# Optimization experiments

Measured on AMD Instinct MI355X. Metric: run time of the kernel, lower is better.

## Reference

```python
import jax, jax.numpy as jnp
import numpy as np

NUM_ANCHORS = 400_000
NUM_GTS = 64
NUM_CLASSES = 1
TOPK = 10
ALPHA = 1.0
BETA = 6.0
IMG = 640.0


def setup_inputs() -> dict:
    key = jax.random.key(0)
    k1, k2, k3, k4, k5, k6 = jax.random.split(key, 6)
    # anchor points uniformly over the image plane
    anc_points = jax.random.uniform(k1, (NUM_ANCHORS, 2), jnp.float32, 0.0, IMG)
    # predicted boxes: centered near the anchor point, valid xyxy
    pd_wh = jax.random.uniform(k2, (NUM_ANCHORS, 2), jnp.float32, 8.0, 96.0)
    pd_bboxes = jnp.concatenate([anc_points - pd_wh * 0.5, anc_points + pd_wh * 0.5], axis=-1)
    # predicted class scores in [0, 1] (post-sigmoid)
    pd_scores = jax.random.uniform(k3, (NUM_ANCHORS, NUM_CLASSES), jnp.float32)
    # GT boxes: random centers / sizes, valid xyxy
    gt_c = jax.random.uniform(k4, (NUM_GTS, 2), jnp.float32, 64.0, IMG - 64.0)
    gt_wh = jax.random.uniform(k5, (NUM_GTS, 2), jnp.float32, 16.0, 128.0)
    gt_bboxes = jnp.concatenate([gt_c - gt_wh * 0.5, gt_c + gt_wh * 0.5], axis=-1)
    gt_labels = jax.random.randint(k6, (NUM_GTS,), 0, NUM_CLASSES, dtype=jnp.int32)
    return {
        "pd_scores": pd_scores,
        "pd_bboxes": pd_bboxes,
        "anc_points": anc_points,
        "gt_labels": gt_labels,
        "gt_bboxes": gt_bboxes,
    }


def _box_iou(b1, b2):
    # b1: [A,4] xyxy, b2: [G,4] xyxy -> [A,G] pairwise IoU (torchvision box_iou math)
    lt = jnp.maximum(b1[:, None, :2], b2[None, :, :2])  # [A,G,2]
    rb = jnp.minimum(b1[:, None, 2:], b2[None, :, 2:])  # [A,G,2]
    wh = jnp.clip(rb - lt, 0.0)
    inter = wh[..., 0] * wh[..., 1]                      # [A,G]
    area1 = (b1[:, 2] - b1[:, 0]) * (b1[:, 3] - b1[:, 1])
    area2 = (b2[:, 2] - b2[:, 0]) * (b2[:, 3] - b2[:, 1])
    return inter / (area1[:, None] + area2[None, :] - inter)


def reference(pd_scores, pd_bboxes, anc_points, gt_labels, gt_bboxes):
    A = anc_points.shape[0]
    G = gt_bboxes.shape[0]
    # is anchor point inside each GT box -> [A,G] bool
    x, y = anc_points[:, 0:1], anc_points[:, 1:2]
    is_in_gts = ((x >= gt_bboxes[None, :, 0]) & (x <= gt_bboxes[None, :, 2]) &
                 (y >= gt_bboxes[None, :, 1]) & (y <= gt_bboxes[None, :, 3]))
    # Original gathers candidate anchors (inside >=1 GT) then computes metrics.
    # Equivalent dense form: non-candidates have is_in_gts row all-False so their
    # alignment metric is 0 for every GT and they are filtered by metric>0 below.
    iou = _box_iou(pd_bboxes, gt_bboxes)                         # [A,G]
    cls_scores = pd_scores[:, gt_labels]                          # [A,G]
    cls_scores = cls_scores * is_in_gts.astype(cls_scores.dtype)
    metric = (cls_scores ** ALPHA) * (iou ** BETA)                # [A,G]
    # per-GT top-k anchors by alignment metric
    _, topk_idx = jax.lax.top_k(metric.T, TOPK)                   # [G,k]
    topk_mask = jnp.zeros((A, G), dtype=bool)
    topk_mask = topk_mask.at[topk_idx.T, jnp.arange(G)[None, :]].set(True)
    topk_mask = topk_mask & (metric > 0)
    is_assigned = topk_mask.any(axis=1)                           # [A]
    best_gt = jnp.argmax(metric, axis=1)                          # [A]
    fg_mask = is_assigned
    assigned_gt_idx = jnp.where(fg_mask, best_gt, 0).astype(jnp.int32)
    return fg_mask, assigned_gt_idx
```

## Files before the change

kernel.cpp:

```cpp
#include <hip/hip_runtime.h>

#define NUM_A    400000
#define NUM_G    64
#define TOPK     10
#define CHUNKS   64
#define CHUNK_SZ (NUM_A / CHUNKS)
#define GGROUP   4
#define NGROUPS  (NUM_G / GGROUP)
#define CAP      768
#define SENT_I   0x7fffffff

__device__ __forceinline__ bool better(float m1, int a1, float m2, int a2) {
    return (m1 > m2) || ((m1 == m2) && (a1 < a2));
}

__device__ __forceinline__ float iou_metric(
    float px1, float py1, float px2, float py2, float parea, float score,
    float gx1, float gy1, float gx2, float gy2, float garea)
{
    float ltx = fmaxf(px1, gx1);
    float lty = fmaxf(py1, gy1);
    float rbx = fminf(px2, gx2);
    float rby = fminf(py2, gy2);
    float w = fmaxf(rbx - ltx, 0.0f);
    float h = fmaxf(rby - lty, 0.0f);
    float inter = w * h;
    float iou = inter / (parea + garea - inter);
    float iou2 = iou * iou;
    float iou6 = iou2 * iou2 * iou2;
    return score * iou6;
}

__device__ __forceinline__ void wave_max_pair(float& bv, int& bi) {
#pragma unroll
    for (int s = 1; s < 64; s <<= 1) {
        float ov = __shfl_xor(bv, s, 64);
        int   oi = __shfl_xor(bi, s, 64);
        if (better(ov, oi, bv, bi)) { bv = ov; bi = oi; }
    }
}

__global__ __launch_bounds__(256) void topk_partial_kernel(
    const float* __restrict__ pd_scores,
    const float* __restrict__ pd_bboxes,
    const float* __restrict__ anc_points,
    const float* __restrict__ gt_bboxes,
    float* __restrict__ pval,
    int*   __restrict__ pidx,
    int*   __restrict__ out_zero)
{
    const int c   = blockIdx.x;
    const int gg  = blockIdx.y;
    const int tid = threadIdx.x;
    const int g0  = gg * GGROUP;

    {
        const int t = (gg * CHUNKS + c) * 256 + tid;
        if (t < (2 * NUM_A) / 4) ((int4*)out_zero)[t] = make_int4(0, 0, 0, 0);
    }

    __shared__ int s_cnt[GGROUP];
    __shared__ int s_cand[GGROUP][CAP];

    if (tid < GGROUP) s_cnt[tid] = 0;

    float gx1[GGROUP], gy1[GGROUP], gx2[GGROUP], gy2[GGROUP];
#pragma unroll
    for (int j = 0; j < GGROUP; ++j) {
        float4 gb = ((const float4*)gt_bboxes)[g0 + j];
        gx1[j] = gb.x; gy1[j] = gb.y; gx2[j] = gb.z; gy2[j] = gb.w;
    }
    __syncthreads();

    const int lane = tid & 63;
    const unsigned long long lmlt = (1ull << lane) - 1ull;

    const int p0 = c * (CHUNK_SZ / 2);
    const int p1 = p0 + CHUNK_SZ / 2;
    for (int p = p0 + tid; p < p1; p += 256) {
        float4 aq = ((const float4*)anc_points)[p];
        const int a2 = 2 * p;
#pragma unroll
        for (int j = 0; j < GGROUP; ++j) {
            bool in0 = (aq.x >= gx1[j]) && (aq.x <= gx2[j]) &&
                       (aq.y >= gy1[j]) && (aq.y <= gy2[j]);
            bool in1 = (aq.z >= gx1[j]) && (aq.z <= gx2[j]) &&
                       (aq.w >= gy1[j]) && (aq.w <= gy2[j]);
            unsigned long long b0 = __ballot(in0);
            unsigned long long b1 = __ballot(in1);
            if (b0 | b1) {
                int c0  = __popcll(b0);
                int tot = c0 + __popcll(b1);
                int base;
                if (lane == 0) base = atomicAdd(&s_cnt[j], tot);
                base = __shfl(base, 0, 64);
                if (in0) {
                    int q = base + __popcll(b0 & lmlt);
                    if (q < CAP) s_cand[j][q] = a2;
                }
                if (in1) {
                    int q = base + c0 + __popcll(b1 & lmlt);
                    if (q < CAP) s_cand[j][q] = a2 + 1;
                }
            }
        }
    }
    __syncthreads();

    const int wj = tid >> 6;

    float4 gb = ((const float4*)gt_bboxes)[g0 + wj];
    const float garea = (gb.z - gb.x) * (gb.w - gb.y);
    const int n = min(s_cnt[wj], CAP);

    float tv[TOPK]; int ti[TOPK];
#pragma unroll
    for (int k = 0; k < TOPK; ++k) { tv[k] = 0.0f; ti[k] = SENT_I; }

    for (int i = lane; i < n; i += 64) {
        const int a = s_cand[wj][i];
        float4 pb = ((const float4*)pd_bboxes)[a];
        float sc = pd_scores[a];
        float parea = (pb.z - pb.x) * (pb.w - pb.y);
        float m = iou_metric(pb.x, pb.y, pb.z, pb.w, parea, sc,
                             gb.x, gb.y, gb.z, gb.w, garea);
        if (better(m, a, tv[TOPK - 1], ti[TOPK - 1])) {
#pragma unroll
            for (int k = TOPK - 1; k >= 1; --k) {
                bool gp = better(m, a, tv[k - 1], ti[k - 1]);
                bool gc = better(m, a, tv[k],     ti[k]);
                tv[k] = gp ? tv[k - 1] : (gc ? m : tv[k]);
                ti[k] = gp ? ti[k - 1] : (gc ? a : ti[k]);
            }
            if (better(m, a, tv[0], ti[0])) { tv[0] = m; ti[0] = a; }
        }
    }

    float outv = 0.0f; int outi = SENT_I;
#pragma unroll
    for (int k = 0; k < TOPK; ++k) {
        float bv = tv[0]; int bi = ti[0];
        wave_max_pair(bv, bi);
        bool win = (ti[0] == bi);
#pragma unroll
        for (int j = 0; j < TOPK - 1; ++j) {
            tv[j] = win ? tv[j + 1] : tv[j];
            ti[j] = win ? ti[j + 1] : ti[j];
        }
        if (win) { tv[TOPK - 1] = 0.0f; ti[TOPK - 1] = SENT_I; }
        if (lane == k) { outv = bv; outi = bi; }
    }
    if (lane < TOPK) {
        const int g = g0 + wj;
        pval[(g * CHUNKS + c) * TOPK + lane] = outv;
        pidx[(g * CHUNKS + c) * TOPK + lane] = outi;
    }
}

__global__ __launch_bounds__(64) void merge_assign_kernel(
    const float* __restrict__ pval,
    const int*   __restrict__ pidx,
    const float* __restrict__ pd_scores,
    const float* __restrict__ pd_bboxes,
    const float* __restrict__ anc_points,
    const float* __restrict__ gt_bboxes,
    int* __restrict__ out_fg,
    int* __restrict__ out_idx)
{
    const int g    = blockIdx.x;
    const int lane = threadIdx.x;

    float4 mygt = ((const float4*)gt_bboxes)[lane];
    float  myga = (mygt.z - mygt.x) * (mygt.w - mygt.y);

    float tv[TOPK]; int ti[TOPK];
    const float* pv = pval + (g * CHUNKS + lane) * TOPK;
    const int*   pi = pidx + (g * CHUNKS + lane) * TOPK;
#pragma unroll
    for (int k = 0; k < TOPK; ++k) { tv[k] = pv[k]; ti[k] = pi[k]; }

    float outv = 0.0f; int outi = SENT_I;
#pragma unroll
    for (int k = 0; k < TOPK; ++k) {
        float bv = tv[0]; int bi = ti[0];
        wave_max_pair(bv, bi);
        bool win = (ti[0] == bi);
#pragma unroll
        for (int j = 0; j < TOPK - 1; ++j) {
            tv[j] = win ? tv[j + 1] : tv[j];
            ti[j] = win ? ti[j + 1] : ti[j];
        }
        if (win) { tv[TOPK - 1] = 0.0f; ti[TOPK - 1] = SENT_I; }
        if (lane == k) { outv = bv; outi = bi; }
    }

    float wv[TOPK]; int wa[TOPK];
#pragma unroll
    for (int k = 0; k < TOPK; ++k) {
        wv[k] = __shfl(outv, k, 64);
        wa[k] = __shfl(outi, k, 64);
    }

    float4 pb[TOPK]; float sc[TOPK]; float2 ap[TOPK];
#pragma unroll
    for (int k = 0; k < TOPK; ++k) {
        const int a = (wv[k] > 0.0f) ? wa[k] : 0;
        pb[k] = ((const float4*)pd_bboxes)[a];
        sc[k] = pd_scores[a];
        ap[k] = ((const float2*)anc_points)[a];
    }

#pragma unroll
    for (int k = 0; k < TOPK; ++k) {
        if (wv[k] > 0.0f) {
            const int a = wa[k];
            float parea = (pb[k].z - pb[k].x) * (pb[k].w - pb[k].y);
            bool in = (ap[k].x >= mygt.x) && (ap[k].x <= mygt.z) &&
                      (ap[k].y >= mygt.y) && (ap[k].y <= mygt.w);
            float m = iou_metric(pb[k].x, pb[k].y, pb[k].z, pb[k].w, parea,
                                 in ? sc[k] : 0.0f,
                                 mygt.x, mygt.y, mygt.z, mygt.w, myga);
            float av = m; int ag = lane;
#pragma unroll
            for (int s = 1; s < 64; s <<= 1) {
                float ov = __shfl_xor(av, s, 64);
                int   og = __shfl_xor(ag, s, 64);
                if ((ov > av) || ((ov == av) && (og < ag))) { av = ov; ag = og; }
            }
            if (lane == 0) { out_fg[a] = 1; out_idx[a] = ag; }
        }
    }
}

extern "C" void kernel_launch(void* const* d_in, const int* in_sizes, int n_in,
                              void* d_out, int out_size, void* d_ws, size_t ws_size,
                              hipStream_t stream) {
    const float* pd_scores  = (const float*)d_in[0];
    const float* pd_bboxes  = (const float*)d_in[1];
    const float* anc_points = (const float*)d_in[2];
    const float* gt_bboxes  = (const float*)d_in[4];

    const int npairs = NUM_G * CHUNKS * TOPK;
    float* pval = (float*)d_ws;
    int*   pidx = (int*)(pval + npairs);

    int* out_fg  = (int*)d_out;
    int* out_idx = out_fg + NUM_A;

    dim3 g1(CHUNKS, NGROUPS);
    topk_partial_kernel<<<g1, 256, 0, stream>>>(
        pd_scores, pd_bboxes, anc_points, gt_bboxes, pval, pidx, out_fg);
    merge_assign_kernel<<<NUM_G, 64, 0, stream>>>(
        pval, pidx, pd_scores, pd_bboxes, anc_points, gt_bboxes,
        out_fg, out_idx);
}
```

Measured before the change: 103.6 us.

## Fuse partial top-k and merge-assign kernels via last-block-per-group atomic counter

Merges the two kernels into one. Each block atomically increments a per-GT-group counter, and the last block for a group performs the merge and assignment for its four GTs, using one wave per GT. A global counter tracks which blocks have finished zeroing the output, and the last block spin-waits on it so its writes are not overwritten by another block's zeroing. This removes a kernel launch and the gap between kernels, but adds a memset launch, atomics, a spin-wait that relies on every block being resident or already finished, and a merge phase that now runs on only 16 blocks.

```diff
diff --git a/kernel.cpp b/kernel.cpp
--- a/kernel.cpp
+++ b/kernel.cpp
@@ -7,6 +7,7 @@
 #define CHUNK_SZ (NUM_A / CHUNKS)
 #define GGROUP   4
 #define NGROUPS  (NUM_G / GGROUP)
+#define NBLOCKS  (CHUNKS * NGROUPS)
 #define CAP      768
 #define SENT_I   0x7fffffff
 
@@ -40,27 +41,33 @@
     }
 }
 
-__global__ __launch_bounds__(256) void topk_partial_kernel(
+__global__ __launch_bounds__(256, 4) void fused_assign_kernel(
     const float* __restrict__ pd_scores,
     const float* __restrict__ pd_bboxes,
     const float* __restrict__ anc_points,
     const float* __restrict__ gt_bboxes,
     float* __restrict__ pval,
     int*   __restrict__ pidx,
-    int*   __restrict__ out_zero)
+    int*   __restrict__ grp_cnt,
+    int*   __restrict__ zero_cnt,
+    int*   __restrict__ out_fg,
+    int*   __restrict__ out_idx)
 {
-    const int c   = blockIdx.x;
-    const int gg  = blockIdx.y;
-    const int tid = threadIdx.x;
-    const int g0  = gg * GGROUP;
+    const int c    = blockIdx.x;
+    const int gg   = blockIdx.y;
+    const int tid  = threadIdx.x;
+    const int g0   = gg * GGROUP;
+    const int wj   = tid >> 6;
+    const int lane = tid & 63;
 
     {
         const int t = (gg * CHUNKS + c) * 256 + tid;
-        if (t < (2 * NUM_A) / 4) ((int4*)out_zero)[t] = make_int4(0, 0, 0, 0);
+        if (t < (2 * NUM_A) / 4) ((int4*)out_fg)[t] = make_int4(0, 0, 0, 0);
     }
 
     __shared__ int s_cnt[GGROUP];
     __shared__ int s_cand[GGROUP][CAP];
+    __shared__ int s_last;
 
     if (tid < GGROUP) s_cnt[tid] = 0;
 
@@ -72,7 +79,8 @@
     }
     __syncthreads();
 
-    const int lane = tid & 63;
+    if (tid == 0) { __threadfence(); atomicAdd(zero_cnt, 1); }
+
     const unsigned long long lmlt = (1ull << lane) - 1ull;
 
     const int p0 = c * (CHUNK_SZ / 2);
@@ -107,127 +115,138 @@
     }
     __syncthreads();
 
-    const int wj = tid >> 6;
-
-    float4 gb = ((const float4*)gt_bboxes)[g0 + wj];
-    const float garea = (gb.z - gb.x) * (gb.w - gb.y);
-    const int n = min(s_cnt[wj], CAP);
-
-    float tv[TOPK]; int ti[TOPK];
-#pragma unroll
-    for (int k = 0; k < TOPK; ++k) { tv[k] = 0.0f; ti[k] = SENT_I; }
-
-    for (int i = lane; i < n; i += 64) {
-        const int a = s_cand[wj][i];
-        float4 pb = ((const float4*)pd_bboxes)[a];
-        float sc = pd_scores[a];
-        float parea = (pb.z - pb.x) * (pb.w - pb.y);
-        float m = iou_metric(pb.x, pb.y, pb.z, pb.w, parea, sc,
-                             gb.x, gb.y, gb.z, gb.w, garea);
-        if (better(m, a, tv[TOPK - 1], ti[TOPK - 1])) {
-#pragma unroll
-            for (int k = TOPK - 1; k >= 1; --k) {
-                bool gp = better(m, a, tv[k - 1], ti[k - 1]);
-                bool gc = better(m, a, tv[k],     ti[k]);
-                tv[k] = gp ? tv[k - 1] : (gc ? m : tv[k]);
-                ti[k] = gp ? ti[k - 1] : (gc ? a : ti[k]);
-            }
-            if (better(m, a, tv[0], ti[0])) { tv[0] = m; ti[0] = a; }
-        }
-    }
-
-    float outv = 0.0f; int outi = SENT_I;
-#pragma unroll
-    for (int k = 0; k < TOPK; ++k) {
-        float bv = tv[0]; int bi = ti[0];
-        wave_max_pair(bv, bi);
-        bool win = (ti[0] == bi);
-#pragma unroll
-        for (int j = 0; j < TOPK - 1; ++j) {
-            tv[j] = win ? tv[j + 1] : tv[j];
-            ti[j] = win ? ti[j + 1] : ti[j];
-        }
-        if (win) { tv[TOPK - 1] = 0.0f; ti[TOPK - 1] = SENT_I; }
-        if (lane == k) { outv = bv; outi = bi; }
-    }
-    if (lane < TOPK) {
+    {
+        float4 gb = ((const float4*)gt_bboxes)[g0 + wj];
+        const float garea = (gb.z - gb.x) * (gb.w - gb.y);
+        const int n = min(s_cnt[wj], CAP);
+
+        float tv[TOPK]; int ti[TOPK];
+#pragma unroll
+        for (int k = 0; k < TOPK; ++k) { tv[k] = 0.0f; ti[k] = SENT_I; }
+
+        for (int i = lane; i < n; i += 64) {
+            const int a = s_cand[wj][i];
+            float4 pb = ((const float4*)pd_bboxes)[a];
+            float sc = pd_scores[a];
+            float parea = (pb.z - pb.x) * (pb.w - pb.y);
+            float m = iou_metric(pb.x, pb.y, pb.z, pb.w, parea, sc,
+                                 gb.x, gb.y, gb.z, gb.w, garea);
+            if (better(m, a, tv[TOPK - 1], ti[TOPK - 1])) {
+#pragma unroll
+                for (int k = TOPK - 1; k >= 1; --k) {
+                    bool gp = better(m, a, tv[k - 1], ti[k - 1]);
+                    bool gc = better(m, a, tv[k],     ti[k]);
+                    tv[k] = gp ? tv[k - 1] : (gc ? m : tv[k]);
+                    ti[k] = gp ? ti[k - 1] : (gc ? a : ti[k]);
+                }
+                if (better(m, a, tv[0], ti[0])) { tv[0] = m; ti[0] = a; }
+            }
+        }
+
+        float outv = 0.0f; int outi = SENT_I;
+#pragma unroll
+        for (int k = 0; k < TOPK; ++k) {
+            float bv = tv[0]; int bi = ti[0];
+            wave_max_pair(bv, bi);
+            bool win = (ti[0] == bi);
+#pragma unroll
+            for (int j = 0; j < TOPK - 1; ++j) {
+                tv[j] = win ? tv[j + 1] : tv[j];
+                ti[j] = win ? ti[j + 1] : ti[j];
+            }
+            if (win) { tv[TOPK - 1] = 0.0f; ti[TOPK - 1] = SENT_I; }
+            if (lane == k) { outv = bv; outi = bi; }
+        }
+        if (lane < TOPK) {
+            const int g = g0 + wj;
+            pval[(g * CHUNKS + c) * TOPK + lane] = outv;
+            pidx[(g * CHUNKS + c) * TOPK + lane] = outi;
+        }
+    }
+    __syncthreads();
+
+    if (tid == 0) {
+        __threadfence();
+        int old = atomicAdd(&grp_cnt[gg], 1);
+        int last = (old == CHUNKS - 1);
+        if (last) {
+            while (__hip_atomic_load(zero_cnt, __ATOMIC_ACQUIRE,
+                                     __HIP_MEMORY_SCOPE_AGENT) < NBLOCKS) {
+                __builtin_amdgcn_s_sleep(8);
+            }
+            __threadfence();
+        }
+        s_last = last;
+    }
+    __syncthreads();
+    if (!s_last) return;
+
+    {
         const int g = g0 + wj;
-        pval[(g * CHUNKS + c) * TOPK + lane] = outv;
-        pidx[(g * CHUNKS + c) * TOPK + lane] = outi;
-    }
-}
-
-__global__ __launch_bounds__(64) void merge_assign_kernel(
-    const float* __restrict__ pval,
-    const int*   __restrict__ pidx,
-    const float* __restrict__ pd_scores,
-    const float* __restrict__ pd_bboxes,
-    const float* __restrict__ anc_points,
-    const float* __restrict__ gt_bboxes,
-    int* __restrict__ out_fg,
-    int* __restrict__ out_idx)
-{
-    const int g    = blockIdx.x;
-    const int lane = threadIdx.x;
-
-    float4 mygt = ((const float4*)gt_bboxes)[lane];
-    float  myga = (mygt.z - mygt.x) * (mygt.w - mygt.y);
-
-    float tv[TOPK]; int ti[TOPK];
-    const float* pv = pval + (g * CHUNKS + lane) * TOPK;
-    const int*   pi = pidx + (g * CHUNKS + lane) * TOPK;
-#pragma unroll
-    for (int k = 0; k < TOPK; ++k) { tv[k] = pv[k]; ti[k] = pi[k]; }
-
-    float outv = 0.0f; int outi = SENT_I;
-#pragma unroll
-    for (int k = 0; k < TOPK; ++k) {
-        float bv = tv[0]; int bi = ti[0];
-        wave_max_pair(bv, bi);
-        bool win = (ti[0] == bi);
-#pragma unroll
-        for (int j = 0; j < TOPK - 1; ++j) {
-            tv[j] = win ? tv[j + 1] : tv[j];
-            ti[j] = win ? ti[j + 1] : ti[j];
-        }
-        if (win) { tv[TOPK - 1] = 0.0f; ti[TOPK - 1] = SENT_I; }
-        if (lane == k) { outv = bv; outi = bi; }
-    }
-
-    float wv[TOPK]; int wa[TOPK];
-#pragma unroll
-    for (int k = 0; k < TOPK; ++k) {
-        wv[k] = __shfl(outv, k, 64);
-        wa[k] = __shfl(outi, k, 64);
-    }
-
-    float4 pb[TOPK]; float sc[TOPK]; float2 ap[TOPK];
-#pragma unroll
-    for (int k = 0; k < TOPK; ++k) {
-        const int a = (wv[k] > 0.0f) ? wa[k] : 0;
-        pb[k] = ((const float4*)pd_bboxes)[a];
-        sc[k] = pd_scores[a];
-        ap[k] = ((const float2*)anc_points)[a];
-    }
-
-#pragma unroll
-    for (int k = 0; k < TOPK; ++k) {
-        if (wv[k] > 0.0f) {
-            const int a = wa[k];
-            float parea = (pb[k].z - pb[k].x) * (pb[k].w - pb[k].y);
-            bool in = (ap[k].x >= mygt.x) && (ap[k].x <= mygt.z) &&
-                      (ap[k].y >= mygt.y) && (ap[k].y <= mygt.w);
-            float m = iou_metric(pb[k].x, pb[k].y, pb[k].z, pb[k].w, parea,
-                                 in ? sc[k] : 0.0f,
-                                 mygt.x, mygt.y, mygt.z, mygt.w, myga);
-            float av = m; int ag = lane;
-#pragma unroll
-            for (int s = 1; s < 64; s <<= 1) {
-                float ov = __shfl_xor(av, s, 64);
-                int   og = __shfl_xor(ag, s, 64);
-                if ((ov > av) || ((ov == av) && (og < ag))) { av = ov; ag = og; }
-            }
-            if (lane == 0) { out_fg[a] = 1; out_idx[a] = ag; }
+
+        float4 mygt = ((const float4*)gt_bboxes)[lane];
+        float  myga = (mygt.z - mygt.x) * (mygt.w - mygt.y);
+
+        float tv[TOPK]; int ti[TOPK];
+        const float* pv = pval + (g * CHUNKS + lane) * TOPK;
+        const int*   pi = pidx + (g * CHUNKS + lane) * TOPK;
+#pragma unroll
+        for (int k = 0; k < TOPK; ++k) { tv[k] = pv[k]; ti[k] = pi[k]; }
+
+        float outv = 0.0f; int outi = SENT_I;
+#pragma unroll
+        for (int k = 0; k < TOPK; ++k) {
+            float bv = tv[0]; int bi = ti[0];
+            wave_max_pair(bv, bi);
+            bool win = (ti[0] == bi);
+#pragma unroll
+            for (int j = 0; j < TOPK - 1; ++j) {
+                tv[j] = win ? tv[j + 1] : tv[j];
+                ti[j] = win ? ti[j + 1] : ti[j];
+            }
+            if (win) { tv[TOPK - 1] = 0.0f; ti[TOPK - 1] = SENT_I; }
+            if (lane == k) { outv = bv; outi = bi; }
+        }
+
+        float wv[TOPK]; int wa[TOPK];
+#pragma unroll
+        for (int k = 0; k < TOPK; ++k) {
+            wv[k] = __shfl(outv, k, 64);
+            wa[k] = __shfl(outi, k, 64);
+        }
+
+#pragma unroll
+        for (int kb = 0; kb < TOPK; kb += 5) {
+            float4 pb[5]; float sc[5]; float2 ap[5];
+#pragma unroll
+            for (int u = 0; u < 5; ++u) {
+                const int k = kb + u;
+                const int a = (wv[k] > 0.0f) ? wa[k] : 0;
+                pb[u] = ((const float4*)pd_bboxes)[a];
+                sc[u] = pd_scores[a];
+                ap[u] = ((const float2*)anc_points)[a];
+            }
+#pragma unroll
+            for (int u = 0; u < 5; ++u) {
+                const int k = kb + u;
+                if (wv[k] > 0.0f) {
+                    const int a = wa[k];
+                    float parea = (pb[u].z - pb[u].x) * (pb[u].w - pb[u].y);
+                    bool in = (ap[u].x >= mygt.x) && (ap[u].x <= mygt.z) &&
+                              (ap[u].y >= mygt.y) && (ap[u].y <= mygt.w);
+                    float m = iou_metric(pb[u].x, pb[u].y, pb[u].z, pb[u].w,
+                                         parea, in ? sc[u] : 0.0f,
+                                         mygt.x, mygt.y, mygt.z, mygt.w, myga);
+                    float av = m; int ag = lane;
+#pragma unroll
+                    for (int s = 1; s < 64; s <<= 1) {
+                        float ov = __shfl_xor(av, s, 64);
+                        int   og = __shfl_xor(ag, s, 64);
+                        if ((ov > av) || ((ov == av) && (og < ag))) { av = ov; ag = og; }
+                    }
+                    if (lane == 0) { out_fg[a] = 1; out_idx[a] = ag; }
+                }
+            }
         }
     }
 }
@@ -243,14 +262,15 @@
     const int npairs = NUM_G * CHUNKS * TOPK;
     float* pval = (float*)d_ws;
     int*   pidx = (int*)(pval + npairs);
+    int*   ctrs = pidx + npairs;
 
     int* out_fg  = (int*)d_out;
     int* out_idx = out_fg + NUM_A;
 
-    dim3 g1(CHUNKS, NGROUPS);
-    topk_partial_kernel<<<g1, 256, 0, stream>>>(
-        pd_scores, pd_bboxes, anc_points, gt_bboxes, pval, pidx, out_fg);
-    merge_assign_kernel<<<NUM_G, 64, 0, stream>>>(
-        pval, pidx, pd_scores, pd_bboxes, anc_points, gt_bboxes,
-        out_fg, out_idx);
-}
+    hipMemsetAsync(ctrs, 0, (NGROUPS + 1) * sizeof(int), stream);
+
+    dim3 grid(CHUNKS, NGROUPS);
+    fused_assign_kernel<<<grid, 256, 0, stream>>>(
+        pd_scores, pd_bboxes, anc_points, gt_bboxes,
+        pval, pidx, ctrs, ctrs + NGROUPS, out_fg, out_idx);
+}
```

After: 147.2 us. 42.2% more time.
